# Kernel optimization log

Measured on AMD Instinct MI355X. Metric: run time of the kernel, lower is better.

## Reference

```python
import jax, jax.numpy as jnp
import numpy as np

EPS_B = 1e-4
ROT_W = 1.0
TRANS_W = 1.0
MIN_CORR = 6

B, S, Nq, PS = 8, 4, 1024, 16
H = W = 256


def _patch_centers(Himg, Wimg, Hp, Wp, dtype):
    ys = (jnp.arange(Hp, dtype=dtype) + 0.5) * (Himg / Hp)
    xs = (jnp.arange(Wp, dtype=dtype) + 0.5) * (Wimg / Wp)
    yy, xx = jnp.meshgrid(ys, xs, indexing='ij')
    return jnp.stack([xx, yy], -1).reshape(Hp * Wp, 2)  # [Nq,2] (x,y)


def _dlt_pnp(pts2d, X_obj, Kq, w):
    # Weighted DLT PnP (stand-in for the iterative EProPnP6DoF solver).
    # pts2d [N,2], X_obj [N,3], Kq [3,3], w [N] -> T [4,4]
    N = X_obj.shape[0]
    Xh = jnp.concatenate([X_obj, jnp.ones((N, 1), X_obj.dtype)], -1)  # [N,4]
    u = pts2d[:, :1]
    v = pts2d[:, 1:2]
    z4 = jnp.zeros_like(Xh)
    r1 = jnp.concatenate([Xh, z4, -u * Xh], -1)  # [N,12]
    r2 = jnp.concatenate([z4, Xh, -v * Xh], -1)
    A = jnp.concatenate([r1, r2], 0)             # [2N,12]
    ww = jnp.concatenate([w, w], 0)              # [2N]
    A1, a2 = A[:, :11], A[:, 11]
    Aw = A1 * ww[:, None]
    G = Aw.T @ A1 + 1e-6 * jnp.eye(11, dtype=A.dtype)
    rhs = -(Aw.T @ a2)
    p = jnp.linalg.solve(G, rhs)
    P = jnp.concatenate([p, jnp.ones((1,), p.dtype)]).reshape(3, 4)
    M = jnp.linalg.inv(Kq) @ P
    M = M * jnp.sign(jnp.linalg.det(M[:, :3]))
    U, D, Vt = jnp.linalg.svd(M[:, :3])
    d = jnp.sign(jnp.linalg.det(U @ Vt))
    diag = jnp.stack([jnp.ones_like(d), jnp.ones_like(d), d])
    R = (U * diag[None, :]) @ Vt
    t = M[:, 3] / jnp.mean(D)
    T = jnp.eye(4, dtype=M.dtype)
    return T.at[:3, :3].set(R).at[:3, 3].set(t)


def setup_inputs() -> dict:
    key = jax.random.key(0)
    k1, k2, k3, k4, k5 = jax.random.split(key, 5)
    rng = np.random.default_rng(0)

    def rand_se3(shape, tz):
        A = rng.normal(size=shape + (3, 3))
        Q, _ = np.linalg.qr(A)
        Q = Q * np.linalg.det(Q)[..., None, None]  # det -> +1 for 3x3
        T = np.tile(np.eye(4, dtype=np.float32), shape + (1, 1))
        T[..., :3, :3] = Q
        T[..., :3, 3] = rng.normal(size=shape + (3,)) * 0.1 + np.array([0.0, 0.0, tz])
        return jnp.asarray(T, jnp.float32)

    Kmat = np.tile(np.eye(3, dtype=np.float32), (B, S + 1, 1, 1))
    Kmat[..., 0, 0] = 320.0
    Kmat[..., 1, 1] = 320.0
    Kmat[..., 0, 2] = W / 2.0
    Kmat[..., 1, 2] = H / 2.0

    return {
        'dense_flow': jax.random.normal(k1, (B, S, Nq, 2), jnp.float32),
        'dense_b': jax.random.uniform(k2, (B, S, Nq, PS, PS), jnp.float32),
        'dense_weight': jax.random.uniform(k3, (B, S, Nq, PS, PS), jnp.float32),
        'patch_cls': jax.random.randint(k4, (B, S, Nq), 0, Nq, jnp.int32),
        'K': jnp.asarray(Kmat),
        'poses': rand_se3((B, S + 1), 3.0),
        'gt_pose': rand_se3((B, S), 3.0),
        'template_depth': jax.random.uniform(k5, (B, S, H, W), jnp.float32) * 2.0 + 0.5,
    }


def reference(dense_flow, dense_b, dense_weight, patch_cls, K, poses, gt_pose, template_depth):
    Bb, Ss, N, ps, _ = dense_b.shape
    Hp = int(round(N ** 0.5))
    Wp = Hp
    Himg, Wimg = template_depth.shape[-2], template_depth.shape[-1]

    valid = (patch_cls >= 0) & (patch_cls < N)
    b = jnp.maximum(dense_b, EPS_B)
    w = dense_weight / (b + EPS_B)
    w_patch = w.mean(axis=(-1, -2))                 # [B,S,Nq]

    centers = _patch_centers(Himg, Wimg, Hp, Wp, dense_b.dtype)  # [Nq,2]
    buddy = jnp.clip(patch_cls, 0, N - 1)
    centers_j = centers[buddy]                       # [B,S,Nq,2]
    x_int = jnp.clip(jnp.round(centers_j[..., 0]), 0, Wimg - 1).astype(jnp.int32)
    y_int = jnp.clip(jnp.round(centers_j[..., 1]), 0, Himg - 1).astype(jnp.int32)
    bi = jnp.arange(Bb)[:, None, None]
    si = jnp.arange(Ss)[None, :, None]
    depth_vals = template_depth[bi, si, y_int, x_int]  # [B,S,Nq]

    K_t = K[:, 1:]
    T_m2c = poses[:, 1:]
    Rm = T_m2c[..., :3, :3]
    tm = T_m2c[..., :3, 3]
    Rt = jnp.swapaxes(Rm, -1, -2)
    tinv = -jnp.einsum('bsij,bsj->bsi', Rt, tm)

    fx = K_t[..., 0, 0][..., None]
    fy = K_t[..., 1, 1][..., None]
    cx = K_t[..., 0, 2][..., None]
    cy = K_t[..., 1, 2][..., None]
    xn = (centers_j[..., 0] - cx) / fx
    yn = (centers_j[..., 1] - cy) / fy
    rays = jnp.stack([xn, yn, jnp.ones_like(xn)], -1)   # [B,S,Nq,3]
    X_cam = rays * depth_vals[..., None]
    X_obj = jnp.einsum('bsij,bsnj->bsni', Rt, X_cam) + tinv[:, :, None, :]

    mask = valid & (w_patch > 0)
    w_eff = jnp.where(mask, w_patch, 0.0).astype(dense_b.dtype)
    pts2d = jnp.broadcast_to(centers, (Bb, Ss, N, 2))
    Kq = jnp.broadcast_to(K[:, 0][:, None], (Bb, Ss, 3, 3))

    T_pred = jax.vmap(jax.vmap(_dlt_pnp))(pts2d, X_obj, Kq, w_eff)  # [B,S,4,4]

    R_pred = T_pred[..., :3, :3]
    t_pred = T_pred[..., :3, 3]
    R_gt = gt_pose[..., :3, :3]
    t_gt = gt_pose[..., :3, 3]
    R_diff = jnp.einsum('bsij,bskj->bsik', R_pred, R_gt)
    trace = jnp.trace(R_diff, axis1=-2, axis2=-1)
    cos_angle = jnp.clip((trace - 1.0) / 2.0, -1.0 + 1e-7, 1.0 - 1e-7)
    rot_err = jnp.arccos(cos_angle)
    trans_err = jnp.linalg.norm(t_pred - t_gt, axis=-1)
    per_sample = ROT_W * rot_err + TRANS_W * trans_err  # [B,S]

    contrib = (mask.sum(-1) >= MIN_CORR).astype(per_sample.dtype)
    count = jnp.maximum(contrib.sum(), 1.0)
    return jnp.sum(per_sample * contrib) / count
```

## Files before the change

### kernel.cpp

```cpp
#include <hip/hip_runtime.h>
#include <math.h>

namespace {

constexpr int Bb = 8, Ss = 4, Nq = 1024, PSq = 256;
constexpr int Himg = 256, Wimg = 256;
constexpr float EPS_B = 1e-4f;
constexpr int MIN_CORR = 6;
constexpr int NBS = Bb * Ss;
constexpr int MOM_STRIDE = 48;

__device__ constexpr int tidx4(int i, int j) {
  const int a = i < j ? i : j;
  const int b = i < j ? j : i;
  return a * 4 - a * (a - 1) / 2 + (b - a);
}

__device__ inline double det3(const double A[3][3]) {
  return A[0][0] * (A[1][1] * A[2][2] - A[1][2] * A[2][1])
       - A[0][1] * (A[1][0] * A[2][2] - A[1][2] * A[2][0])
       + A[0][2] * (A[1][0] * A[2][1] - A[1][1] * A[2][0]);
}

__global__ __launch_bounds__(256) void wpatch_kernel(
    const float* __restrict__ db, const float* __restrict__ dw,
    float* __restrict__ wpatch)
{
  const int lane = threadIdx.x & 63;
  const int wv   = threadIdx.x >> 6;
  const int p    = blockIdx.x * 4 + wv;
  const float4 bv  = reinterpret_cast<const float4*>(db + (size_t)p * PSq)[lane];
  const float4 wvv = reinterpret_cast<const float4*>(dw + (size_t)p * PSq)[lane];
  float s = wvv.x / (fmaxf(bv.x, EPS_B) + EPS_B)
          + wvv.y / (fmaxf(bv.y, EPS_B) + EPS_B)
          + wvv.z / (fmaxf(bv.z, EPS_B) + EPS_B)
          + wvv.w / (fmaxf(bv.w, EPS_B) + EPS_B);
  #pragma unroll
  for (int off = 32; off > 0; off >>= 1) s += __shfl_down(s, off);
  if (lane == 0) wpatch[p] = s * (1.0f / 256.0f);
}

__global__ __launch_bounds__(256) void moments_kernel(
    const float* __restrict__ wpatch,
    const int*   __restrict__ patch_cls,
    const float* __restrict__ K,
    const float* __restrict__ poses,
    const float* __restrict__ depth,
    double* __restrict__ mom)
{
  const int bs = blockIdx.x;
  const int b  = bs / Ss;
  const int s  = bs - b * Ss;
  const int tid = threadIdx.x;

  const float* Kt = K + ((size_t)b * (Ss + 1) + (1 + s)) * 9;
  const double fx = Kt[0], cx = Kt[2], fy = Kt[4], cy = Kt[5];
  const float* Tm = poses + ((size_t)b * (Ss + 1) + (1 + s)) * 16;
  double Rt[3][3], tinv[3];
  #pragma unroll
  for (int i = 0; i < 3; i++)
    #pragma unroll
    for (int j = 0; j < 3; j++) Rt[i][j] = (double)Tm[j * 4 + i];
  {
    const double t0 = Tm[3], t1 = Tm[7], t2 = Tm[11];
    #pragma unroll
    for (int i = 0; i < 3; i++)
      tinv[i] = -(Rt[i][0] * t0 + Rt[i][1] * t1 + Rt[i][2] * t2);
  }

  double acc[40];
  #pragma unroll
  for (int a = 0; a < 40; a++) acc[a] = 0.0;
  int mcount = 0;

  const float* dimg = depth + (size_t)bs * Himg * Wimg;
  for (int n = tid; n < Nq; n += 256) {
    const int pc   = patch_cls[(size_t)bs * Nq + n];
    const float wp = wpatch[(size_t)bs * Nq + n];
    const bool mask = (pc >= 0) && (pc < Nq) && (wp > 0.0f);
    mcount += mask ? 1 : 0;
    const double w = mask ? (double)wp : 0.0;
    const int buddy = min(max(pc, 0), Nq - 1);
    const int xj = (buddy & 31) * 8 + 4;
    const int yj = (buddy >> 5) * 8 + 4;
    const double dep = (double)dimg[yj * Wimg + xj];
    const double xn = ((double)xj - cx) / fx;
    const double yn = ((double)yj - cy) / fy;
    const double Xc = xn * dep, Yc = yn * dep, Zc = dep;
    const double h0 = Rt[0][0] * Xc + Rt[0][1] * Yc + Rt[0][2] * Zc + tinv[0];
    const double h1 = Rt[1][0] * Xc + Rt[1][1] * Yc + Rt[1][2] * Zc + tinv[1];
    const double h2 = Rt[2][0] * Xc + Rt[2][1] * Yc + Rt[2][2] * Zc + tinv[2];
    const double u = (double)((n & 31) * 8 + 4);
    const double v = (double)((n >> 5) * 8 + 4);
    const double h[4] = {h0, h1, h2, 1.0};
    const double wu = w * u, wvw = w * v, wuv = w * (u * u + v * v);
    int k = 0;
    #pragma unroll
    for (int i = 0; i < 4; i++)
      #pragma unroll
      for (int j = i; j < 4; j++) {
        const double hh = h[i] * h[j];
        acc[k]      += w   * hh;
        acc[10 + k] += wu  * hh;
        acc[20 + k] += wvw * hh;
        acc[30 + k] += wuv * hh;
        k++;
      }
  }

  __shared__ double red[4][41];
  const int lane = tid & 63, wid = tid >> 6;
  #pragma unroll
  for (int a = 0; a < 40; a++) {
    double x = acc[a];
    for (int off = 32; off > 0; off >>= 1) x += __shfl_down(x, off);
    if (lane == 0) red[wid][a] = x;
  }
  {
    int m = mcount;
    for (int off = 32; off > 0; off >>= 1) m += __shfl_down(m, off);
    if (lane == 0) red[wid][40] = (double)m;
  }
  __syncthreads();
  if (tid < 41)
    mom[(size_t)bs * MOM_STRIDE + tid] =
        red[0][tid] + red[1][tid] + red[2][tid] + red[3][tid];
}

__global__ __launch_bounds__(64, 1) void solve_finalize_kernel(
    const double* __restrict__ mom,
    const float* __restrict__ K,
    const float* __restrict__ gt_pose,
    float* __restrict__ out)
{
  const int lane = threadIdx.x;
  double per = 0.0;
  float ctr = 0.0f;

  if (lane < NBS) {
    const int bs = lane;
    const int b  = bs / Ss;

    double S[41];
    #pragma unroll
    for (int a = 0; a < 41; a++) S[a] = mom[(size_t)bs * MOM_STRIDE + a];
    const int mtot = (int)(S[40] + 0.5);
    const double* M0f  = S;
    const double* Muf  = S + 10;
    const double* Mvf  = S + 20;
    const double* Muvf = S + 30;

    auto Gel = [&](int i, int j) -> double {
      if (i > j) { const int t = i; i = j; j = t; }
      double g;
      if (j < 4) {
        g = M0f[tidx4(i, j)];
      } else if (j < 8) {
        g = (i < 4) ? 0.0 : M0f[tidx4(i - 4, j - 4)];
      } else {
        if (i < 4)      g = -Muf[tidx4(i, j - 8)];
        else if (i < 8) g = -Mvf[tidx4(i - 4, j - 8)];
        else            g = Muvf[tidx4(i - 8, j - 8)];
      }
      if (i == j) g += 1e-6;
      return g;
    };

    double A[66], rhs[11];
    #pragma unroll
    for (int i = 0; i < 11; i++) {
      #pragma unroll
      for (int j = 0; j <= i; j++) A[i * (i + 1) / 2 + j] = Gel(i, j);
      rhs[i] = (i < 4) ? Muf[tidx4(i, 3)]
             : (i < 8) ? Mvf[tidx4(i - 4, 3)]
                       : -Muvf[tidx4(i - 8, 3)];
    }
    #pragma unroll
    for (int j = 0; j < 11; j++) {
      double d = A[j * (j + 1) / 2 + j];
      #pragma unroll
      for (int k = 0; k < j; k++) {
        const double l = A[j * (j + 1) / 2 + k];
        d -= l * l;
      }
      d = sqrt(d);
      A[j * (j + 1) / 2 + j] = d;
      const double inv = 1.0 / d;
      #pragma unroll
      for (int i = j + 1; i < 11; i++) {
        double sv = A[i * (i + 1) / 2 + j];
        #pragma unroll
        for (int k = 0; k < j; k++)
          sv -= A[i * (i + 1) / 2 + k] * A[j * (j + 1) / 2 + k];
        A[i * (i + 1) / 2 + j] = sv * inv;
      }
    }
    #pragma unroll
    for (int i = 0; i < 11; i++) {
      double sv = rhs[i];
      #pragma unroll
      for (int k = 0; k < i; k++) sv -= A[i * (i + 1) / 2 + k] * rhs[k];
      rhs[i] = sv / A[i * (i + 1) / 2 + i];
    }
    #pragma unroll
    for (int ii = 10; ii >= 0; ii--) {
      double sv = rhs[ii];
      #pragma unroll
      for (int k = ii + 1; k < 11; k++) sv -= A[k * (k + 1) / 2 + ii] * rhs[k];
      rhs[ii] = sv / A[ii * (ii + 1) / 2 + ii];
    }

    const double P3[3][4] = {{rhs[0], rhs[1], rhs[2],  rhs[3]},
                             {rhs[4], rhs[5], rhs[6],  rhs[7]},
                             {rhs[8], rhs[9], rhs[10], 1.0}};
    const float* Kq = K + (size_t)b * (Ss + 1) * 9;
    const double k00 = Kq[0], k01 = Kq[1], k02 = Kq[2];
    const double k10 = Kq[3], k11 = Kq[4], k12 = Kq[5];
    const double k20 = Kq[6], k21 = Kq[7], k22 = Kq[8];
    const double dK = k00 * (k11 * k22 - k12 * k21) - k01 * (k10 * k22 - k12 * k20)
                    + k02 * (k10 * k21 - k11 * k20);
    const double iK[3][3] = {
      {(k11 * k22 - k12 * k21) / dK, (k02 * k21 - k01 * k22) / dK, (k01 * k12 - k02 * k11) / dK},
      {(k12 * k20 - k10 * k22) / dK, (k00 * k22 - k02 * k20) / dK, (k02 * k10 - k00 * k12) / dK},
      {(k10 * k21 - k11 * k20) / dK, (k01 * k20 - k00 * k21) / dK, (k00 * k11 - k01 * k10) / dK}};
    double M[3][4];
    #pragma unroll
    for (int i = 0; i < 3; i++)
      #pragma unroll
      for (int j = 0; j < 4; j++)
        M[i][j] = iK[i][0] * P3[0][j] + iK[i][1] * P3[1][j] + iK[i][2] * P3[2][j];
    double M3[3][3];
    #pragma unroll
    for (int i = 0; i < 3; i++)
      #pragma unroll
      for (int j = 0; j < 3; j++) M3[i][j] = M[i][j];
    const double dm = det3(M3);
    const double sgn = (dm > 0.0) ? 1.0 : ((dm < 0.0) ? -1.0 : 0.0);
    #pragma unroll
    for (int i = 0; i < 3; i++) {
      #pragma unroll
      for (int j = 0; j < 4; j++) M[i][j] *= sgn;
      #pragma unroll
      for (int j = 0; j < 3; j++) M3[i][j] *= sgn;
    }

    double Am[3][3], Vm[3][3] = {{1, 0, 0}, {0, 1, 0}, {0, 0, 1}};
    #pragma unroll
    for (int i = 0; i < 3; i++)
      #pragma unroll
      for (int j = 0; j < 3; j++) Am[i][j] = M3[i][j];
    for (int sweep = 0; sweep < 10; sweep++) {
      #pragma unroll
      for (int pr = 0; pr < 3; pr++) {
        const int pp = (pr == 2) ? 1 : 0;
        const int qq = (pr == 0) ? 1 : 2;
        double al = 0.0, be = 0.0, ga = 0.0;
        #pragma unroll
        for (int i = 0; i < 3; i++) {
          al += Am[i][pp] * Am[i][pp];
          be += Am[i][qq] * Am[i][qq];
          ga += Am[i][pp] * Am[i][qq];
        }
        if (ga != 0.0) {
          const double tau = (be - al) / (2.0 * ga);
          const double tt = -((tau >= 0.0) ? 1.0 : -1.0) /
                            (fabs(tau) + sqrt(1.0 + tau * tau));
          const double c = 1.0 / sqrt(1.0 + tt * tt), sn = tt * c;
          #pragma unroll
          for (int i = 0; i < 3; i++) {
            const double ap = Am[i][pp], aq = Am[i][qq];
            Am[i][pp] = c * ap + sn * aq; Am[i][qq] = -sn * ap + c * aq;
            const double vp = Vm[i][pp], vq = Vm[i][qq];
            Vm[i][pp] = c * vp + sn * vq; Vm[i][qq] = -sn * vp + c * vq;
          }
        }
      }
    }
    double sig[3];
    #pragma unroll
    for (int j = 0; j < 3; j++)
      sig[j] = sqrt(Am[0][j] * Am[0][j] + Am[1][j] * Am[1][j] + Am[2][j] * Am[2][j]);
    #pragma unroll
    for (int a = 0; a < 3; a++)
      #pragma unroll
      for (int jj = 0; jj < 2; jj++)
        if (sig[jj] < sig[jj + 1]) {
          double tq = sig[jj]; sig[jj] = sig[jj + 1]; sig[jj + 1] = tq;
          #pragma unroll
          for (int i = 0; i < 3; i++) {
            tq = Am[i][jj]; Am[i][jj] = Am[i][jj + 1]; Am[i][jj + 1] = tq;
            tq = Vm[i][jj]; Vm[i][jj] = Vm[i][jj + 1]; Vm[i][jj + 1] = tq;
          }
        }
    double U[3][3];
    #pragma unroll
    for (int j = 0; j < 3; j++) {
      const double invs = 1.0 / fmax(sig[j], 1e-300);
      #pragma unroll
      for (int i = 0; i < 3; i++) U[i][j] = Am[i][j] * invs;
    }
    const double dd = (det3(U) * det3(Vm) >= 0.0) ? 1.0 : -1.0;
    double R[3][3];
    #pragma unroll
    for (int i = 0; i < 3; i++)
      #pragma unroll
      for (int j = 0; j < 3; j++)
        R[i][j] = U[i][0] * Vm[j][0] + U[i][1] * Vm[j][1] + dd * U[i][2] * Vm[j][2];
    const double meanD = (sig[0] + sig[1] + sig[2]) * (1.0 / 3.0);
    const double tp0 = M[0][3] / meanD, tp1 = M[1][3] / meanD, tp2 = M[2][3] / meanD;

    const float* Tg = gt_pose + (size_t)bs * 16;
    double tr = 0.0;
    #pragma unroll
    for (int i = 0; i < 3; i++)
      #pragma unroll
      for (int j = 0; j < 3; j++) tr += R[i][j] * (double)Tg[i * 4 + j];
    double ca = (tr - 1.0) * 0.5;
    ca = fmin(fmax(ca, -1.0 + 1e-7), 1.0 - 1e-7);
    const double rot = acos(ca);
    const double d0 = tp0 - (double)Tg[3];
    const double d1 = tp1 - (double)Tg[7];
    const double d2 = tp2 - (double)Tg[11];
    ctr = (mtot >= MIN_CORR) ? 1.0f : 0.0f;
    per = (rot + sqrt(d0 * d0 + d1 * d1 + d2 * d2)) * (double)ctr;
  }

  #pragma unroll
  for (int off = 32; off > 0; off >>= 1) {
    per += __shfl_down(per, off);
    ctr += __shfl_down(ctr, off);
  }
  if (lane == 0) out[0] = (float)(per / (double)fmaxf(ctr, 1.0f));
}

}

extern "C" void kernel_launch(void* const* d_in, const int* in_sizes, int n_in,
                              void* d_out, int out_size, void* d_ws, size_t ws_size,
                              hipStream_t stream) {
  const float* dense_b      = (const float*)d_in[1];
  const float* dense_weight = (const float*)d_in[2];
  const int*   patch_cls    = (const int*)d_in[3];
  const float* K            = (const float*)d_in[4];
  const float* poses        = (const float*)d_in[5];
  const float* gt           = (const float*)d_in[6];
  const float* depth        = (const float*)d_in[7];

  float*  wpatch = (float*)d_ws;
  double* mom    = (double*)((char*)d_ws + (size_t)NBS * Nq * sizeof(float));

  wpatch_kernel<<<dim3(NBS * Nq / 4), dim3(256), 0, stream>>>(dense_b, dense_weight, wpatch);
  moments_kernel<<<dim3(NBS), dim3(256), 0, stream>>>(wpatch, patch_cls, K, poses, depth, mom);
  solve_finalize_kernel<<<dim3(1), dim3(64), 0, stream>>>(mom, K, gt, (float*)d_out);
}
```

Measured before the change: 154.3 us.

## Fuse patch-weight reduction into moments kernel with split partial sums

Merges the per-patch weight kernel and the moments kernel into one kernel launched as 16 blocks per (batch, sample). Each block reduces 64 patches' weights into shared memory, then one wavefront computes moment contributions and writes per-block partials. The finalize kernel now sums the 16 partials per sample. This removes a kernel launch and the global round trip for the weights, and spreads the moment work over more blocks, at the cost of more partial-sum traffic and three waves idling in the moment phase.

```diff
diff --git a/kernel.cpp b/kernel.cpp
--- a/kernel.cpp
+++ b/kernel.cpp
@@ -8,7 +8,9 @@
 constexpr float EPS_B = 1e-4f;
 constexpr int MIN_CORR = 6;
 constexpr int NBS = Bb * Ss;
-constexpr int MOM_STRIDE = 48;
+constexpr int BLOCKS_PER_BS = 16;
+constexpr int PATCHES_PER_BLOCK = Nq / BLOCKS_PER_BS;
+constexpr int PART_STRIDE = 48;
 
 __device__ constexpr int tidx4(int i, int j) {
   const int a = i < j ? i : j;
@@ -22,67 +24,64 @@
        + A[0][2] * (A[1][0] * A[2][1] - A[1][1] * A[2][0]);
 }
 
-__global__ __launch_bounds__(256) void wpatch_kernel(
+__global__ __launch_bounds__(256, 2) void fused_moments_kernel(
     const float* __restrict__ db, const float* __restrict__ dw,
-    float* __restrict__ wpatch)
-{
-  const int lane = threadIdx.x & 63;
-  const int wv   = threadIdx.x >> 6;
-  const int p    = blockIdx.x * 4 + wv;
-  const float4 bv  = reinterpret_cast<const float4*>(db + (size_t)p * PSq)[lane];
-  const float4 wvv = reinterpret_cast<const float4*>(dw + (size_t)p * PSq)[lane];
-  float s = wvv.x / (fmaxf(bv.x, EPS_B) + EPS_B)
-          + wvv.y / (fmaxf(bv.y, EPS_B) + EPS_B)
-          + wvv.z / (fmaxf(bv.z, EPS_B) + EPS_B)
-          + wvv.w / (fmaxf(bv.w, EPS_B) + EPS_B);
-  #pragma unroll
-  for (int off = 32; off > 0; off >>= 1) s += __shfl_down(s, off);
-  if (lane == 0) wpatch[p] = s * (1.0f / 256.0f);
-}
-
-__global__ __launch_bounds__(256) void moments_kernel(
-    const float* __restrict__ wpatch,
     const int*   __restrict__ patch_cls,
     const float* __restrict__ K,
     const float* __restrict__ poses,
     const float* __restrict__ depth,
-    double* __restrict__ mom)
+    double* __restrict__ part)
 {
-  const int bs = blockIdx.x;
-  const int b  = bs / Ss;
-  const int s  = bs - b * Ss;
-  const int tid = threadIdx.x;
-
-  const float* Kt = K + ((size_t)b * (Ss + 1) + (1 + s)) * 9;
-  const double fx = Kt[0], cx = Kt[2], fy = Kt[4], cy = Kt[5];
-  const float* Tm = poses + ((size_t)b * (Ss + 1) + (1 + s)) * 16;
-  double Rt[3][3], tinv[3];
+  const int blk   = blockIdx.x;
+  const int bs    = blk / BLOCKS_PER_BS;
+  const int chunk = blk - bs * BLOCKS_PER_BS;
+  const int tid   = threadIdx.x;
+  const int lane  = tid & 63, wv = tid >> 6;
+
+  __shared__ float lds_w[PATCHES_PER_BLOCK];
+
+  const size_t patch_base = (size_t)bs * Nq + (size_t)chunk * PATCHES_PER_BLOCK;
   #pragma unroll
-  for (int i = 0; i < 3; i++)
-    #pragma unroll
-    for (int j = 0; j < 3; j++) Rt[i][j] = (double)Tm[j * 4 + i];
-  {
-    const double t0 = Tm[3], t1 = Tm[7], t2 = Tm[11];
-    #pragma unroll
-    for (int i = 0; i < 3; i++)
-      tinv[i] = -(Rt[i][0] * t0 + Rt[i][1] * t1 + Rt[i][2] * t2);
+  for (int i = 0; i < PATCHES_PER_BLOCK / 4; i++) {
+    const int pl = wv * (PATCHES_PER_BLOCK / 4) + i;
+    const size_t off = (patch_base + pl) * PSq + (size_t)lane * 4;
+    const float4 bv  = *reinterpret_cast<const float4*>(db + off);
+    const float4 wvv = *reinterpret_cast<const float4*>(dw + off);
+    float s = wvv.x / (fmaxf(bv.x, EPS_B) + EPS_B)
+            + wvv.y / (fmaxf(bv.y, EPS_B) + EPS_B)
+            + wvv.z / (fmaxf(bv.z, EPS_B) + EPS_B)
+            + wvv.w / (fmaxf(bv.w, EPS_B) + EPS_B);
+    #pragma unroll
+    for (int o = 32; o > 0; o >>= 1) s += __shfl_down(s, o);
+    if (lane == 0) lds_w[pl] = s * (1.0f / 256.0f);
   }
-
-  double acc[40];
-  #pragma unroll
-  for (int a = 0; a < 40; a++) acc[a] = 0.0;
-  int mcount = 0;
-
-  const float* dimg = depth + (size_t)bs * Himg * Wimg;
-  for (int n = tid; n < Nq; n += 256) {
+  __syncthreads();
+
+  if (wv == 0) {
+    const float* Kt = K + ((size_t)bs / Ss * (Ss + 1) + 1 + (bs % Ss)) * 9;
+    const double fx = Kt[0], cx = Kt[2], fy = Kt[4], cy = Kt[5];
+    const float* Tm = poses + ((size_t)(bs / Ss) * (Ss + 1) + 1 + (bs % Ss)) * 16;
+    double Rt[3][3], tinv[3];
+    #pragma unroll
+    for (int i = 0; i < 3; i++)
+      #pragma unroll
+      for (int j = 0; j < 3; j++) Rt[i][j] = (double)Tm[j * 4 + i];
+    {
+      const double t0 = Tm[3], t1 = Tm[7], t2 = Tm[11];
+      #pragma unroll
+      for (int i = 0; i < 3; i++)
+        tinv[i] = -(Rt[i][0] * t0 + Rt[i][1] * t1 + Rt[i][2] * t2);
+    }
+
+    const int n = chunk * PATCHES_PER_BLOCK + lane;
     const int pc   = patch_cls[(size_t)bs * Nq + n];
-    const float wp = wpatch[(size_t)bs * Nq + n];
+    const float wp = lds_w[lane];
     const bool mask = (pc >= 0) && (pc < Nq) && (wp > 0.0f);
-    mcount += mask ? 1 : 0;
     const double w = mask ? (double)wp : 0.0;
     const int buddy = min(max(pc, 0), Nq - 1);
     const int xj = (buddy & 31) * 8 + 4;
     const int yj = (buddy >> 5) * 8 + 4;
+    const float* dimg = depth + (size_t)bs * Himg * Wimg;
     const double dep = (double)dimg[yj * Wimg + xj];
     const double xn = ((double)xj - cx) / fx;
     const double yn = ((double)yj - cy) / fy;
@@ -94,41 +93,39 @@
     const double v = (double)((n >> 5) * 8 + 4);
     const double h[4] = {h0, h1, h2, 1.0};
     const double wu = w * u, wvw = w * v, wuv = w * (u * u + v * v);
+
+    double m[41];
     int k = 0;
     #pragma unroll
     for (int i = 0; i < 4; i++)
       #pragma unroll
       for (int j = i; j < 4; j++) {
         const double hh = h[i] * h[j];
-        acc[k]      += w   * hh;
-        acc[10 + k] += wu  * hh;
-        acc[20 + k] += wvw * hh;
-        acc[30 + k] += wuv * hh;
+        m[k]      = w   * hh;
+        m[10 + k] = wu  * hh;
+        m[20 + k] = wvw * hh;
+        m[30 + k] = wuv * hh;
         k++;
       }
+    m[40] = mask ? 1.0 : 0.0;
+
+    #pragma unroll
+    for (int a = 0; a < 41; a++) {
+      double x = m[a];
+      #pragma unroll
+      for (int o = 32; o > 0; o >>= 1) x += __shfl_down(x, o);
+      m[a] = x;
+    }
+    if (lane == 0) {
+      double* p = part + (size_t)blk * PART_STRIDE;
+      #pragma unroll
+      for (int a = 0; a < 41; a++) p[a] = m[a];
+    }
   }
-
-  __shared__ double red[4][41];
-  const int lane = tid & 63, wid = tid >> 6;
-  #pragma unroll
-  for (int a = 0; a < 40; a++) {
-    double x = acc[a];
-    for (int off = 32; off > 0; off >>= 1) x += __shfl_down(x, off);
-    if (lane == 0) red[wid][a] = x;
-  }
-  {
-    int m = mcount;
-    for (int off = 32; off > 0; off >>= 1) m += __shfl_down(m, off);
-    if (lane == 0) red[wid][40] = (double)m;
-  }
-  __syncthreads();
-  if (tid < 41)
-    mom[(size_t)bs * MOM_STRIDE + tid] =
-        red[0][tid] + red[1][tid] + red[2][tid] + red[3][tid];
 }
 
 __global__ __launch_bounds__(64, 1) void solve_finalize_kernel(
-    const double* __restrict__ mom,
+    const double* __restrict__ part,
     const float* __restrict__ K,
     const float* __restrict__ gt_pose,
     float* __restrict__ out)
@@ -143,7 +140,13 @@
 
     double S[41];
     #pragma unroll
-    for (int a = 0; a < 41; a++) S[a] = mom[(size_t)bs * MOM_STRIDE + a];
+    for (int a = 0; a < 41; a++) S[a] = 0.0;
+    #pragma unroll
+    for (int c = 0; c < BLOCKS_PER_BS; c++) {
+      const double* p = part + ((size_t)bs * BLOCKS_PER_BS + c) * PART_STRIDE;
+      #pragma unroll
+      for (int a = 0; a < 41; a++) S[a] += p[a];
+    }
     const int mtot = (int)(S[40] + 0.5);
     const double* M0f  = S;
     const double* Muf  = S + 10;
@@ -346,10 +349,9 @@
   const float* gt           = (const float*)d_in[6];
   const float* depth        = (const float*)d_in[7];
 
-  float*  wpatch = (float*)d_ws;
-  double* mom    = (double*)((char*)d_ws + (size_t)NBS * Nq * sizeof(float));
-
-  wpatch_kernel<<<dim3(NBS * Nq / 4), dim3(256), 0, stream>>>(dense_b, dense_weight, wpatch);
-  moments_kernel<<<dim3(NBS), dim3(256), 0, stream>>>(wpatch, patch_cls, K, poses, depth, mom);
-  solve_finalize_kernel<<<dim3(1), dim3(64), 0, stream>>>(mom, K, gt, (float*)d_out);
-}
+  double* part = (double*)d_ws;
+
+  fused_moments_kernel<<<dim3(NBS * BLOCKS_PER_BS), dim3(256), 0, stream>>>(
+      dense_b, dense_weight, patch_cls, K, poses, depth, part);
+  solve_finalize_kernel<<<dim3(1), dim3(64), 0, stream>>>(part, K, gt, (float*)d_out);
+}
```

After: 139.8 us. 9.4% less time.
